# Kernel optimization log

Measured on AMD Instinct MI355X. Metric: run time of the kernel, lower is better.

The kernel has to match this reference:

```python
import jax, jax.numpy as jnp
import numpy as np

BS, L, D, CACHE = 8, 2048, 2048, 64   # sequences, tokens/seq, embed_dim, cache rows
T = BS * L
EPS = 1e-6


def setup_inputs() -> dict:
    key = jax.random.key(0)
    ks = jax.random.split(key, 7)
    inputs = jax.random.normal(ks[0], (T, D), jnp.float32)
    lf1_caches = jax.random.normal(ks[1], (CACHE, D), jnp.float32)
    lf2_caches = jax.random.normal(ks[2], (CACHE, D // 2), jnp.float32)
    conv1_weight = jax.random.normal(ks[3], (D, D), jnp.float32) * 0.02
    conv2_weight = jax.random.normal(ks[4], (D // 2, 2 * D), jnp.float32) * 0.02
    conv1_bias = jax.random.normal(ks[5], (D // 2,), jnp.float32) * 0.02
    conv2_bias = jax.random.normal(ks[6], (D,), jnp.float32) * 0.02
    ln_weight = jnp.ones((D,), jnp.float32)
    # consistent continuous-batching layout: each sequence s occupies rows
    # [s*(L+1) .. s*(L+1)+L] of the padded buffer: [cache_tok, tok0..tok_{L-1}]
    s = np.arange(BS, dtype=np.int64)
    j = np.arange(L, dtype=np.int64)
    pre_lf_indexs = jnp.asarray(s)                                  # cache slot per seq
    out_lf_indexs = jnp.asarray(s)
    input_lf_loc = jnp.asarray(s * (L + 1))                         # where cache row goes
    out_lf_loc = jnp.asarray(s * (L + 1) + L)                       # last token -> cache
    inputs_loc = jnp.asarray((s[:, None] * (L + 1) + 1 + j[None, :]).reshape(-1))
    outputs_loc = jnp.asarray((s[:, None] * (L + 1) + j[None, :]).reshape(-1))
    return {
        "inputs": inputs, "pre_lf_indexs": pre_lf_indexs, "out_lf_indexs": out_lf_indexs,
        "input_lf_loc": input_lf_loc, "out_lf_loc": out_lf_loc,
        "inputs_loc": inputs_loc, "outputs_loc": outputs_loc,
        "lf1_caches": lf1_caches, "lf2_caches": lf2_caches,
        "conv1_weight": conv1_weight, "conv2_weight": conv2_weight,
        "conv1_bias": conv1_bias, "conv2_bias": conv2_bias, "ln_weight": ln_weight,
    }


def _fused_cat_conv2d(x, cache, pre_idx, in_lf_loc, in_loc, out_loc, W):
    # scatter tokens + gathered cache rows into padded buffer [T+bs, d]
    bs = pre_idx.shape[0]
    xt = jnp.zeros((x.shape[0] + bs, x.shape[1]), x.dtype)
    xt = xt.at[in_loc].set(x).at[in_lf_loc].set(cache[pre_idx])
    c = xt @ W                                  # [T+bs, 2h]
    h = c.shape[1] // 2
    y = c[:-1, :h] + c[1:, h:]                  # kernel-2 causal conv via shift-add
    return y[out_loc]                           # [T, h]


def reference(inputs, pre_lf_indexs, out_lf_indexs, input_lf_loc, out_lf_loc,
              inputs_loc, outputs_loc, lf1_caches, lf2_caches,
              conv1_weight, conv2_weight, conv1_bias, conv2_bias, ln_weight):
    o1 = _fused_cat_conv2d(inputs, lf1_caches, pre_lf_indexs, input_lf_loc,
                           inputs_loc, outputs_loc, conv1_weight) + conv1_bias
    o2 = _fused_cat_conv2d(o1, lf2_caches, pre_lf_indexs, input_lf_loc,
                           inputs_loc, outputs_loc, conv2_weight) + conv2_bias
    o3 = o2 + inputs
    var = jnp.mean(o3 * o3, axis=-1, keepdims=True)          # RMSNorm
    return o3 * jax.lax.rsqrt(var + EPS) * ln_weight
```

## Files before the change

kernel.cpp:

```cpp
#include <hip/hip_runtime.h>
#include <hip/hip_bf16.h>
#include <stdint.h>

#define T_TOK   16384
#define BSQ     8
#define D1      2048
#define D2      1024

typedef __attribute__((ext_vector_type(8))) short bf16x8;
typedef __attribute__((ext_vector_type(4))) float f32x4;

__device__ __forceinline__ void gll16(const void* g, void* l) {
  __builtin_amdgcn_global_load_lds(
      (const __attribute__((address_space(1))) void*)g,
      (__attribute__((address_space(3))) void*)l, 16, 0, 0);
}

__global__ __launch_bounds__(256) void transpose_all(
    const float* __restrict__ W1, const float* __restrict__ W2,
    __hip_bfloat16* __restrict__ bt1, __hip_bfloat16* __restrict__ bt2) {
  __shared__ float tile[32][33];
  int job = blockIdx.x >> 11;
  int i = blockIdx.x & 2047;
  const float* in; __hip_bfloat16* out;
  int Cin, ldout, c0, kout0, bx, by;
  if (job < 2) {
    in = W1; out = bt1; Cin = 2048; ldout = 4096;
    c0 = job ? 1024 : 0; kout0 = job ? 2048 : 0;
    bx = (i & 31) * 32; by = (i >> 5) * 32;
  } else {
    in = W2; out = bt2; Cin = 4096; ldout = 2048;
    c0 = (job == 3) ? 2048 : 0; kout0 = (job == 3) ? 1024 : 0;
    bx = (i & 63) * 32; by = (i >> 6) * 32;
  }
  int tx = threadIdx.x, ty = threadIdx.y;
  #pragma unroll
  for (int q = 0; q < 32; q += 8)
    tile[ty + q][tx] = in[(size_t)(by + ty + q) * Cin + c0 + bx + tx];
  __syncthreads();
  #pragma unroll
  for (int q = 0; q < 32; q += 8)
    out[(size_t)(bx + ty + q) * ldout + kout0 + by + tx] =
        __float2bfloat16(tile[tx][ty + q]);
}

__global__ __launch_bounds__(256) void prologue(
    const float* __restrict__ x, const int* __restrict__ loc,
    const float* __restrict__ lf1, const float* __restrict__ lf2,
    const int* __restrict__ pre, const int* __restrict__ lfloc,
    __hip_bfloat16* __restrict__ xt1, __hip_bfloat16* __restrict__ xt2) {
  int b = blockIdx.x;
  if (b < T_TOK) {
    int c = threadIdx.x * 8;
    int r = loc[b];
    const float* src = x + (size_t)b * 2048 + c;
    float4 v0 = *(const float4*)src;
    float4 v1 = *(const float4*)(src + 4);
    union { __hip_bfloat16 h[8]; uint4 u; } o;
    o.h[0] = __float2bfloat16(v0.x); o.h[1] = __float2bfloat16(v0.y);
    o.h[2] = __float2bfloat16(v0.z); o.h[3] = __float2bfloat16(v0.w);
    o.h[4] = __float2bfloat16(v1.x); o.h[5] = __float2bfloat16(v1.y);
    o.h[6] = __float2bfloat16(v1.z); o.h[7] = __float2bfloat16(v1.w);
    *(uint4*)(xt1 + (size_t)r * 2048 + c) = o.u;
  } else if (b < T_TOK + BSQ) {
    int s = b - T_TOK;
    int dst = lfloc[s];
    const float* src = lf1 + (size_t)pre[s] * 2048;
    for (int c = threadIdx.x; c < 2048; c += 256)
      xt1[(size_t)dst * 2048 + c] = __float2bfloat16(src[c]);
  } else {
    int s = b - T_TOK - BSQ;
    int dst = lfloc[s];
    const float* src = lf2 + (size_t)pre[s] * 1024;
    for (int c = threadIdx.x; c < 1024; c += 256)
      xt2[(size_t)dst * 1024 + c] = __float2bfloat16(src[c]);
  }
}

template <int EPI>
__global__ __launch_bounds__(512, 2) void gemm_conv256(
    const __hip_bfloat16* __restrict__ A0,
    const __hip_bfloat16* __restrict__ Bt,
    const float* __restrict__ bias,
    const float* __restrict__ resid,
    __hip_bfloat16* __restrict__ outb,
    float* __restrict__ outf,
    int N, int K, int KH, int ldA, int tnBits) {
  extern __shared__ char smem[];
  const int tid = threadIdx.x;
  const int wave = tid >> 6, lane = tid & 63;
  const int wm = wave & 1, wn = wave >> 1;

  const int nwg = gridDim.x;
  const int bid = blockIdx.x;
  const int lb = (bid & 7) * (nwg >> 3) + (bid >> 3);
  const int tn = lb & ((1 << tnBits) - 1);
  const int tm = lb >> tnBits;

  const int s = tm >> 3;
  const size_t r0 = (size_t)tm * 256 + s;
  const int NTH = KH >> 6;
  const int NT = NTH * 2;

  const __hip_bfloat16* Bb = Bt + (size_t)tn * 256 * K;

  const int rloc = tid >> 3;
  const int c8 = (((tid & 7) ^ (rloc & 7)) << 3);

  const int frow = lane & 15;
  const int xr = (lane & 7) << 3;
  const int fk = (lane >> 4) << 3;
  const int ek0 = fk ^ xr;
  const int ek1 = (fk | 32) ^ xr;
  int aoff[8], boff[4];
  #pragma unroll
  for (int i = 0; i < 8; ++i) aoff[i] = (wm * 128 + i * 16 + frow) * 64;
  #pragma unroll
  for (int j = 0; j < 4; ++j) boff[j] = (wn * 64 + j * 16 + frow) * 64;

  f32x4 acc[8][4];
  #pragma unroll
  for (int i = 0; i < 8; ++i)
    #pragma unroll
    for (int j = 0; j < 4; ++j)
      #pragma unroll
      for (int e = 0; e < 4; ++e) acc[i][j][e] = 0.0f;

  auto stage = [&](int buf, int t) {
    int seg = (t >= NTH) ? 1 : 0;
    int kk = (t - (seg ? NTH : 0)) << 6;
    const __hip_bfloat16* Ar = A0 + (r0 + seg) * (size_t)ldA + kk + c8;
    const __hip_bfloat16* Bs = Bb + (seg ? KH : 0) + kk + c8;
    char* sbase = smem + buf * 65536 + wave * 1024;
    #pragma unroll
    for (int h = 0; h < 2; ++h)
      #pragma unroll
      for (int l = 0; l < 2; ++l) {
        int grow = h * 128 + l * 64 + rloc;
        gll16(Ar + (size_t)grow * ldA, sbase + h * 16384 + l * 8192);
        gll16(Bs + (size_t)grow * K,   sbase + 32768 + h * 16384 + l * 8192);
      }
  };

  stage(0, 0);
  stage(1, 1);
  asm volatile("s_waitcnt vmcnt(8)" ::: "memory");
  __builtin_amdgcn_s_barrier();
  asm volatile("" ::: "memory");

  #pragma unroll 1
  for (int t = 0; t < NT; t += 2) {
    #pragma unroll
    for (int half = 0; half < 2; ++half) {
      const int tt = t + half;
      const __hip_bfloat16* sT = (const __hip_bfloat16*)(smem + half * 65536);
      const __hip_bfloat16* sB = sT + 16384;

      __builtin_amdgcn_s_setprio(1);
      #pragma unroll
      for (int k = 0; k < 2; ++k) {
        const int ek = k ? ek1 : ek0;
        bf16x8 b[4], a[8];
        #pragma unroll
        for (int j = 0; j < 4; ++j) b[j] = *(const bf16x8*)(sB + boff[j] + ek);
        #pragma unroll
        for (int i = 0; i < 8; ++i) a[i] = *(const bf16x8*)(sT + aoff[i] + ek);
        #pragma unroll
        for (int i = 0; i < 8; ++i)
          #pragma unroll
          for (int j = 0; j < 4; ++j)
            acc[i][j] = __builtin_amdgcn_mfma_f32_16x16x32_bf16(
                a[i], b[j], acc[i][j], 0, 0, 0);
      }
      __builtin_amdgcn_s_setprio(0);

      asm volatile("s_waitcnt lgkmcnt(0)" ::: "memory");
      __builtin_amdgcn_s_barrier();
      asm volatile("" ::: "memory");

      if (tt + 2 < NT) {
        stage(half, tt + 2);
        __builtin_amdgcn_sched_barrier(0);
        asm volatile("s_waitcnt vmcnt(8)" ::: "memory");
      } else {
        asm volatile("s_waitcnt vmcnt(0)" ::: "memory");
      }
      __builtin_amdgcn_s_barrier();
      asm volatile("" ::: "memory");
    }
  }

  const int t0 = tm * 256 + wm * 128 + ((lane >> 4) << 2);
  const int ccol = tn * 256 + wn * 64 + (lane & 15);
  float bj[4];
  #pragma unroll
  for (int j = 0; j < 4; ++j) bj[j] = bias[ccol + j * 16];

  #pragma unroll
  for (int i = 0; i < 8; ++i)
    #pragma unroll
    for (int p = 0; p < 4; ++p) {
      int tk = t0 + i * 16 + p;
      if (EPI == 1) {
        __hip_bfloat16* dst = outb + ((size_t)tk + s + 1) * N + ccol;
        #pragma unroll
        for (int j = 0; j < 4; ++j)
          dst[j * 16] = __float2bfloat16(acc[i][j][p] + bj[j]);
      } else {
        const float* rsrc = resid + (size_t)tk * N + ccol;
        float* dst = outf + (size_t)tk * N + ccol;
        #pragma unroll
        for (int j = 0; j < 4; ++j)
          dst[j * 16] = acc[i][j][p] + bj[j] + rsrc[j * 16];
      }
    }
}

__global__ __launch_bounds__(256) void rmsnorm(
    const float* __restrict__ o3, const float* __restrict__ lnw,
    float* __restrict__ out) {
  __shared__ float red[4];
  int t = blockIdx.x;
  int d = threadIdx.x * 8;
  const float* p = o3 + (size_t)t * 2048 + d;
  float o[8];
  *(float4*)&o[0] = *(const float4*)p;
  *(float4*)&o[4] = *(const float4*)(p + 4);
  float ss = 0.0f;
  #pragma unroll
  for (int k = 0; k < 8; ++k) ss += o[k] * o[k];
  #pragma unroll
  for (int off = 32; off > 0; off >>= 1) ss += __shfl_down(ss, off, 64);
  if ((threadIdx.x & 63) == 0) red[threadIdx.x >> 6] = ss;
  __syncthreads();
  float tot = red[0] + red[1] + red[2] + red[3];
  float sc = rsqrtf(tot * (1.0f / 2048.0f) + 1e-6f);
  float lw[8], res[8];
  *(float4*)&lw[0] = *(const float4*)(lnw + d);
  *(float4*)&lw[4] = *(const float4*)(lnw + d + 4);
  #pragma unroll
  for (int k = 0; k < 8; ++k) res[k] = o[k] * sc * lw[k];
  float* dst = out + (size_t)t * 2048 + d;
  *(float4*)dst = *(float4*)&res[0];
  *(float4*)(dst + 4) = *(float4*)&res[4];
}

extern "C" void kernel_launch(void* const* d_in, const int* in_sizes, int n_in,
                              void* d_out, int out_size, void* d_ws, size_t ws_size,
                              hipStream_t stream) {
  const float* inputs = (const float*)d_in[0];
  const int* pre_idx  = (const int*)d_in[1];
  const int* in_lf_loc = (const int*)d_in[3];
  const int* in_loc  = (const int*)d_in[5];
  const float* lf1 = (const float*)d_in[7];
  const float* lf2 = (const float*)d_in[8];
  const float* W1 = (const float*)d_in[9];
  const float* W2 = (const float*)d_in[10];
  const float* b1 = (const float*)d_in[11];
  const float* b2 = (const float*)d_in[12];
  const float* lnw = (const float*)d_in[13];
  float* out = (float*)d_out;

  char* ws = (char*)d_ws;
  float* o3 = (float*)ws;
  __hip_bfloat16* xt1 = (__hip_bfloat16*)(ws + 134217728ull);
  __hip_bfloat16* xt2 = (__hip_bfloat16*)(ws + 201359360ull);
  __hip_bfloat16* bt1 = (__hip_bfloat16*)(ws + 234930176ull);
  __hip_bfloat16* bt2 = (__hip_bfloat16*)(ws + 243318784ull);

  static int lds_inited = 0;
  if (!lds_inited) {
    lds_inited = 1;
    (void)hipFuncSetAttribute(reinterpret_cast<const void*>(&gemm_conv256<1>),
                              hipFuncAttributeMaxDynamicSharedMemorySize, 131072);
    (void)hipFuncSetAttribute(reinterpret_cast<const void*>(&gemm_conv256<2>),
                              hipFuncAttributeMaxDynamicSharedMemorySize, 131072);
  }

  transpose_all<<<8192, dim3(32, 8), 0, stream>>>(W1, W2, bt1, bt2);
  prologue<<<T_TOK + 2 * BSQ, 256, 0, stream>>>(
      inputs, in_loc, lf1, lf2, pre_idx, in_lf_loc, xt1, xt2);

  gemm_conv256<1><<<256, 512, 131072, stream>>>(
      xt1, bt1, b1, nullptr, xt2, nullptr, 1024, 4096, 2048, 2048, 2);

  gemm_conv256<2><<<512, 512, 131072, stream>>>(
      xt2, bt2, b2, inputs, nullptr, o3, 2048, 2048, 1024, 1024, 3);

  rmsnorm<<<T_TOK, 256, 0, stream>>>(o3, lnw, out);
}
```

Before: 575.8 us.

## Restructure GEMM main loop into finer-grained interleaved load/compute phases

Splits each K-tile's compute into four sub-phases of 16 MFMAs. The global-to-LDS staging of the next tile's A and B quarters is issued between them, with barriers around each sub-phase, in the style of an 8-wave ping-pong schedule. The aim is to spread memory traffic across the compute and hide load latency better than the previous two-stage all-at-once staging. In exchange it adds many more barriers per iteration and tighter vmcnt waits, which could serialize waves if the overlap does not pay off.

```diff
diff --git a/kernel.cpp b/kernel.cpp
--- a/kernel.cpp
+++ b/kernel.cpp
@@ -107,6 +107,29 @@
   const int rloc = tid >> 3;
   const int c8 = (((tid & 7) ^ (rloc & 7)) << 3);
 
+  auto stageA = [&](int buf, int t, int qsel) {
+    int seg = (t >= NTH) ? 1 : 0;
+    int kk = (t - (seg ? NTH : 0)) << 6;
+    const __hip_bfloat16* Ar = A0 + (r0 + seg) * (size_t)ldA + kk + c8;
+    char* sb = smem + buf * 65536 + (size_t)(qsel * 64 + wave * 8) * 128;
+    #pragma unroll
+    for (int l = 0; l < 2; ++l) {
+      int grow = l * 128 + qsel * 64 + rloc;
+      gll16(Ar + (size_t)grow * ldA, sb + l * 16384);
+    }
+  };
+  auto stageB = [&](int buf, int t, int hsel) {
+    int seg = (t >= NTH) ? 1 : 0;
+    int kk = (t - (seg ? NTH : 0)) << 6;
+    const __hip_bfloat16* Bs = Bb + (seg ? KH : 0) + kk + c8;
+    char* sb = smem + buf * 65536 + 32768 + (size_t)(hsel * 128 + wave * 8) * 128;
+    #pragma unroll
+    for (int l = 0; l < 2; ++l) {
+      int grow = hsel * 128 + l * 64 + rloc;
+      gll16(Bs + (size_t)grow * K, sb + l * 8192);
+    }
+  };
+
   const int frow = lane & 15;
   const int xr = (lane & 7) << 3;
   const int fk = (lane >> 4) << 3;
@@ -126,68 +149,99 @@
       #pragma unroll
       for (int e = 0; e < 4; ++e) acc[i][j][e] = 0.0f;
 
-  auto stage = [&](int buf, int t) {
-    int seg = (t >= NTH) ? 1 : 0;
-    int kk = (t - (seg ? NTH : 0)) << 6;
-    const __hip_bfloat16* Ar = A0 + (r0 + seg) * (size_t)ldA + kk + c8;
-    const __hip_bfloat16* Bs = Bb + (seg ? KH : 0) + kk + c8;
-    char* sbase = smem + buf * 65536 + wave * 1024;
-    #pragma unroll
-    for (int h = 0; h < 2; ++h)
-      #pragma unroll
-      for (int l = 0; l < 2; ++l) {
-        int grow = h * 128 + l * 64 + rloc;
-        gll16(Ar + (size_t)grow * ldA, sbase + h * 16384 + l * 8192);
-        gll16(Bs + (size_t)grow * K,   sbase + 32768 + h * 16384 + l * 8192);
-      }
-  };
-
-  stage(0, 0);
-  stage(1, 1);
-  asm volatile("s_waitcnt vmcnt(8)" ::: "memory");
+  stageA(0, 0, 0);
+  stageA(0, 0, 1);
+  stageB(0, 0, 0);
+  stageB(0, 0, 1);
+  stageA(1, 1, 0);
+  asm volatile("s_waitcnt vmcnt(2)" ::: "memory");
   __builtin_amdgcn_s_barrier();
   asm volatile("" ::: "memory");
 
   #pragma unroll 1
-  for (int t = 0; t < NT; t += 2) {
-    #pragma unroll
-    for (int half = 0; half < 2; ++half) {
-      const int tt = t + half;
-      const __hip_bfloat16* sT = (const __hip_bfloat16*)(smem + half * 65536);
-      const __hip_bfloat16* sB = sT + 16384;
-
-      __builtin_amdgcn_s_setprio(1);
-      #pragma unroll
-      for (int k = 0; k < 2; ++k) {
-        const int ek = k ? ek1 : ek0;
-        bf16x8 b[4], a[8];
-        #pragma unroll
-        for (int j = 0; j < 4; ++j) b[j] = *(const bf16x8*)(sB + boff[j] + ek);
-        #pragma unroll
-        for (int i = 0; i < 8; ++i) a[i] = *(const bf16x8*)(sT + aoff[i] + ek);
-        #pragma unroll
-        for (int i = 0; i < 8; ++i)
-          #pragma unroll
-          for (int j = 0; j < 4; ++j)
-            acc[i][j] = __builtin_amdgcn_mfma_f32_16x16x32_bf16(
-                a[i], b[j], acc[i][j], 0, 0, 0);
-      }
-      __builtin_amdgcn_s_setprio(0);
-
-      asm volatile("s_waitcnt lgkmcnt(0)" ::: "memory");
-      __builtin_amdgcn_s_barrier();
-      asm volatile("" ::: "memory");
-
-      if (tt + 2 < NT) {
-        stage(half, tt + 2);
-        __builtin_amdgcn_sched_barrier(0);
-        asm volatile("s_waitcnt vmcnt(8)" ::: "memory");
-      } else {
-        asm volatile("s_waitcnt vmcnt(0)" ::: "memory");
-      }
-      __builtin_amdgcn_s_barrier();
-      asm volatile("" ::: "memory");
-    }
+  for (int v = 0; v < NT; ++v) {
+    const int p = v & 1;
+    const __hip_bfloat16* sA_ = (const __hip_bfloat16*)(smem + p * 65536);
+    const __hip_bfloat16* sB_ = sA_ + 16384;
+    bf16x8 a[4], b[4];
+
+    #pragma unroll
+    for (int j = 0; j < 4; ++j) b[j] = *(const bf16x8*)(sB_ + boff[j] + ek0);
+    #pragma unroll
+    for (int i = 0; i < 4; ++i) a[i] = *(const bf16x8*)(sA_ + aoff[i] + ek0);
+    if (v + 1 < NT) stageA(p ^ 1, v + 1, 1);
+    asm volatile("" ::: "memory");
+    __builtin_amdgcn_s_barrier();
+    asm volatile("s_waitcnt lgkmcnt(0)" ::: "memory");
+    __builtin_amdgcn_sched_barrier(0);
+    __builtin_amdgcn_s_setprio(1);
+    #pragma unroll
+    for (int i = 0; i < 4; ++i)
+      #pragma unroll
+      for (int j = 0; j < 4; ++j)
+        acc[i][j] = __builtin_amdgcn_mfma_f32_16x16x32_bf16(a[i], b[j], acc[i][j], 0, 0, 0);
+    __builtin_amdgcn_s_setprio(0);
+    asm volatile("" ::: "memory");
+    __builtin_amdgcn_s_barrier();
+    asm volatile("" ::: "memory");
+
+    #pragma unroll
+    for (int i = 0; i < 4; ++i) a[i] = *(const bf16x8*)(sA_ + aoff[4 + i] + ek0);
+    if (v + 1 < NT) stageB(p ^ 1, v + 1, 0);
+    asm volatile("" ::: "memory");
+    __builtin_amdgcn_s_barrier();
+    asm volatile("s_waitcnt lgkmcnt(0)" ::: "memory");
+    __builtin_amdgcn_sched_barrier(0);
+    __builtin_amdgcn_s_setprio(1);
+    #pragma unroll
+    for (int i = 0; i < 4; ++i)
+      #pragma unroll
+      for (int j = 0; j < 4; ++j)
+        acc[4 + i][j] = __builtin_amdgcn_mfma_f32_16x16x32_bf16(a[i], b[j], acc[4 + i][j], 0, 0, 0);
+    __builtin_amdgcn_s_setprio(0);
+    asm volatile("" ::: "memory");
+    __builtin_amdgcn_s_barrier();
+    asm volatile("" ::: "memory");
+
+    #pragma unroll
+    for (int j = 0; j < 4; ++j) b[j] = *(const bf16x8*)(sB_ + boff[j] + ek1);
+    #pragma unroll
+    for (int i = 0; i < 4; ++i) a[i] = *(const bf16x8*)(sA_ + aoff[i] + ek1);
+    if (v + 1 < NT) stageB(p ^ 1, v + 1, 1);
+    asm volatile("" ::: "memory");
+    __builtin_amdgcn_s_barrier();
+    asm volatile("s_waitcnt lgkmcnt(0)" ::: "memory");
+    __builtin_amdgcn_sched_barrier(0);
+    __builtin_amdgcn_s_setprio(1);
+    #pragma unroll
+    for (int i = 0; i < 4; ++i)
+      #pragma unroll
+      for (int j = 0; j < 4; ++j)
+        acc[i][j] = __builtin_amdgcn_mfma_f32_16x16x32_bf16(a[i], b[j], acc[i][j], 0, 0, 0);
+    __builtin_amdgcn_s_setprio(0);
+    asm volatile("" ::: "memory");
+    __builtin_amdgcn_s_barrier();
+    asm volatile("" ::: "memory");
+
+    #pragma unroll
+    for (int i = 0; i < 4; ++i) a[i] = *(const bf16x8*)(sA_ + aoff[4 + i] + ek1);
+    if (v + 2 < NT) stageA(p, v + 2, 0);
+    __builtin_amdgcn_sched_barrier(0);
+    if (v < NT - 2) { asm volatile("s_waitcnt vmcnt(2)" ::: "memory"); }
+    else            { asm volatile("s_waitcnt vmcnt(0)" ::: "memory"); }
+    __builtin_amdgcn_s_barrier();
+    asm volatile("s_waitcnt lgkmcnt(0)" ::: "memory");
+    __builtin_amdgcn_sched_barrier(0);
+    __builtin_amdgcn_s_setprio(1);
+    #pragma unroll
+    for (int i = 0; i < 4; ++i)
+      #pragma unroll
+      for (int j = 0; j < 4; ++j)
+        acc[4 + i][j] = __builtin_amdgcn_mfma_f32_16x16x32_bf16(a[i], b[j], acc[4 + i][j], 0, 0, 0);
+    __builtin_amdgcn_s_setprio(0);
+    asm volatile("" ::: "memory");
+    __builtin_amdgcn_s_barrier();
+    asm volatile("" ::: "memory");
   }
 
   const int t0 = tm * 256 + wm * 128 + ((lane >> 4) << 2);
```

Measured after the change: 605.8 us. 5.2% more time.

## Software-pipeline LDS fragment reads against MFMA in GEMM main loop

Applied to the files above, without the earlier changes.

Restructures the GEMM inner loop so LDS fragment reads for the next sub-block are issued while MFMAs on the current sub-block run, splitting A into two M-halves and prefetching the first fragments of the next K tile before the loop iteration ends. Global-to-LDS staging is split into A and B helpers and issued mid-iteration, overlapping with the last MFMA group. This aims to hide LDS read latency behind matrix math. In exchange it raises register pressure from more live fragment buffers and drops the setprio hints.

```diff
diff --git a/kernel.cpp b/kernel.cpp
--- a/kernel.cpp
+++ b/kernel.cpp
@@ -107,6 +107,29 @@
   const int rloc = tid >> 3;
   const int c8 = (((tid & 7) ^ (rloc & 7)) << 3);
 
+  auto stageA = [&](int buf, int t, int qsel) {
+    int seg = (t >= NTH) ? 1 : 0;
+    int kk = (t - (seg ? NTH : 0)) << 6;
+    const __hip_bfloat16* Ar = A0 + (r0 + seg) * (size_t)ldA + kk + c8;
+    char* sb = smem + buf * 65536 + (size_t)(qsel * 64 + wave * 8) * 128;
+    #pragma unroll
+    for (int l = 0; l < 2; ++l) {
+      int grow = l * 128 + qsel * 64 + rloc;
+      gll16(Ar + (size_t)grow * ldA, sb + l * 16384);
+    }
+  };
+  auto stageB = [&](int buf, int t, int hsel) {
+    int seg = (t >= NTH) ? 1 : 0;
+    int kk = (t - (seg ? NTH : 0)) << 6;
+    const __hip_bfloat16* Bs = Bb + (seg ? KH : 0) + kk + c8;
+    char* sb = smem + buf * 65536 + 32768 + (size_t)(hsel * 128 + wave * 8) * 128;
+    #pragma unroll
+    for (int l = 0; l < 2; ++l) {
+      int grow = hsel * 128 + l * 64 + rloc;
+      gll16(Bs + (size_t)grow * K, sb + l * 8192);
+    }
+  };
+
   const int frow = lane & 15;
   const int xr = (lane & 7) << 3;
   const int fk = (lane >> 4) << 3;
@@ -126,67 +149,71 @@
       #pragma unroll
       for (int e = 0; e < 4; ++e) acc[i][j][e] = 0.0f;
 
-  auto stage = [&](int buf, int t) {
-    int seg = (t >= NTH) ? 1 : 0;
-    int kk = (t - (seg ? NTH : 0)) << 6;
-    const __hip_bfloat16* Ar = A0 + (r0 + seg) * (size_t)ldA + kk + c8;
-    const __hip_bfloat16* Bs = Bb + (seg ? KH : 0) + kk + c8;
-    char* sbase = smem + buf * 65536 + wave * 1024;
-    #pragma unroll
-    for (int h = 0; h < 2; ++h)
+  bf16x8 a0[4], a1[4], a2[4], a3[4], b0[4], b1[4];
+
+  auto rdA = [&](bf16x8* d, const __hip_bfloat16* base, int mh, int ek) {
+    #pragma unroll
+    for (int i = 0; i < 4; ++i)
+      d[i] = *(const bf16x8*)(base + aoff[mh * 4 + i] + ek);
+  };
+  auto rdB = [&](bf16x8* d, const __hip_bfloat16* base, int ek) {
+    #pragma unroll
+    for (int j = 0; j < 4; ++j)
+      d[j] = *(const bf16x8*)(base + boff[j] + ek);
+  };
+  auto mm = [&](int mh, const bf16x8* a, const bf16x8* b) {
+    #pragma unroll
+    for (int i = 0; i < 4; ++i)
       #pragma unroll
-      for (int l = 0; l < 2; ++l) {
-        int grow = h * 128 + l * 64 + rloc;
-        gll16(Ar + (size_t)grow * ldA, sbase + h * 16384 + l * 8192);
-        gll16(Bs + (size_t)grow * K,   sbase + 32768 + h * 16384 + l * 8192);
-      }
-  };
-
-  stage(0, 0);
-  stage(1, 1);
+      for (int j = 0; j < 4; ++j)
+        acc[mh * 4 + i][j] = __builtin_amdgcn_mfma_f32_16x16x32_bf16(
+            a[i], b[j], acc[mh * 4 + i][j], 0, 0, 0);
+  };
+
+  stageA(0, 0, 0); stageA(0, 0, 1); stageB(0, 0, 0); stageB(0, 0, 1);
+  stageA(1, 1, 0); stageA(1, 1, 1); stageB(1, 1, 0); stageB(1, 1, 1);
   asm volatile("s_waitcnt vmcnt(8)" ::: "memory");
   __builtin_amdgcn_s_barrier();
   asm volatile("" ::: "memory");
 
+  const __hip_bfloat16* sA_ = (const __hip_bfloat16*)smem;
+  const __hip_bfloat16* sB_ = sA_ + 16384;
+  rdB(b0, sB_, ek0);
+  rdA(a0, sA_, 0, ek0);
+
   #pragma unroll 1
-  for (int t = 0; t < NT; t += 2) {
-    #pragma unroll
-    for (int half = 0; half < 2; ++half) {
-      const int tt = t + half;
-      const __hip_bfloat16* sT = (const __hip_bfloat16*)(smem + half * 65536);
-      const __hip_bfloat16* sB = sT + 16384;
-
-      __builtin_amdgcn_s_setprio(1);
-      #pragma unroll
-      for (int k = 0; k < 2; ++k) {
-        const int ek = k ? ek1 : ek0;
-        bf16x8 b[4], a[8];
-        #pragma unroll
-        for (int j = 0; j < 4; ++j) b[j] = *(const bf16x8*)(sB + boff[j] + ek);
-        #pragma unroll
-        for (int i = 0; i < 8; ++i) a[i] = *(const bf16x8*)(sT + aoff[i] + ek);
-        #pragma unroll
-        for (int i = 0; i < 8; ++i)
-          #pragma unroll
-          for (int j = 0; j < 4; ++j)
-            acc[i][j] = __builtin_amdgcn_mfma_f32_16x16x32_bf16(
-                a[i], b[j], acc[i][j], 0, 0, 0);
-      }
-      __builtin_amdgcn_s_setprio(0);
-
-      asm volatile("s_waitcnt lgkmcnt(0)" ::: "memory");
+  for (int v = 0; v < NT; ++v) {
+    const int p = v & 1;
+
+    rdA(a1, sA_, 1, ek0);
+    mm(0, a0, b0);
+
+    rdB(b1, sB_, ek1);
+    rdA(a2, sA_, 0, ek1);
+    mm(1, a1, b0);
+
+    rdA(a3, sA_, 1, ek1);
+    mm(0, a2, b1);
+
+    asm volatile("s_waitcnt lgkmcnt(0)" ::: "memory");
+    __builtin_amdgcn_s_barrier();
+    asm volatile("" ::: "memory");
+
+    if (v + 2 < NT) {
+      stageA(p, v + 2, 0); stageA(p, v + 2, 1);
+      stageB(p, v + 2, 0); stageB(p, v + 2, 1);
+    }
+    mm(1, a3, b1);
+
+    if (v + 1 < NT) {
+      if (v + 2 < NT) { asm volatile("s_waitcnt vmcnt(8)" ::: "memory"); }
+      else            { asm volatile("s_waitcnt vmcnt(0)" ::: "memory"); }
       __builtin_amdgcn_s_barrier();
       asm volatile("" ::: "memory");
-
-      if (tt + 2 < NT) {
-        stage(half, tt + 2);
-        __builtin_amdgcn_sched_barrier(0);
-        asm volatile("s_waitcnt vmcnt(8)" ::: "memory");
-      } else {
-        asm volatile("s_waitcnt vmcnt(0)" ::: "memory");
-      }
-      __builtin_amdgcn_s_barrier();
-      asm volatile("" ::: "memory");
+      sA_ = (const __hip_bfloat16*)(smem + (p ^ 1) * 65536);
+      sB_ = sA_ + 16384;
+      rdB(b0, sB_, ek0);
+      rdA(a0, sA_, 0, ek0);
     }
   }
 
```

Result: no change. 573.8 us (-0.4%).

## Restructure GEMM to 128x256 tiles with triple-buffered K=32 stages

Applied to the files above, without the earlier changes.

The conv GEMM now uses 256-thread workgroups with 128x256 output tiles and a K step of 32, and twice as many workgroups are launched. LDS goes from two 64 KB buffers to three 24 KB stages with a 3-deep load pipeline, and each stage's fragments are prefetched into registers before the next MFMA loop. The swizzle pattern and per-wave fragment layout are rewritten to match. The aim is better occupancy and latency hiding from the smaller LDS footprint and more workgroups, at the cost of more barriers per unit of K and less reuse per tile.

```diff
diff --git a/kernel.cpp b/kernel.cpp
--- a/kernel.cpp
+++ b/kernel.cpp
@@ -78,7 +78,7 @@
 }
 
 template <int EPI>
-__global__ __launch_bounds__(512, 2) void gemm_conv256(
+__global__ __launch_bounds__(256, 2) void gemm_conv128(
     const __hip_bfloat16* __restrict__ A0,
     const __hip_bfloat16* __restrict__ Bt,
     const float* __restrict__ bias,
@@ -97,120 +97,118 @@
   const int tn = lb & ((1 << tnBits) - 1);
   const int tm = lb >> tnBits;
 
-  const int s = tm >> 3;
-  const size_t r0 = (size_t)tm * 256 + s;
-  const int NTH = KH >> 6;
+  const int s = tm >> 4;
+  const size_t r0 = (size_t)tm * 128 + s;
+  const int NTH = KH >> 5;
   const int NT = NTH * 2;
 
   const __hip_bfloat16* Bb = Bt + (size_t)tn * 256 * K;
 
-  const int rloc = tid >> 3;
-  const int c8 = (((tid & 7) ^ (rloc & 7)) << 3);
+  const int rloc = tid >> 2;
+  const int c8 = (((tid & 3) ^ ((tid >> 3) & 3)) << 3);
+  const int ldsb = wave * 1024;
+
+  auto stage = [&](char* dst, int t) {
+    int seg = (t >= NTH) ? 1 : 0;
+    int kk = (t - (seg ? NTH : 0)) << 5;
+    const __hip_bfloat16* Ar = A0 + (r0 + seg) * (size_t)ldA + kk + c8;
+    const __hip_bfloat16* Bs = Bb + (seg ? KH : 0) + kk + c8;
+    #pragma unroll
+    for (int l = 0; l < 2; ++l)
+      gll16(Ar + (size_t)(l * 64 + rloc) * ldA, dst + l * 4096 + ldsb);
+    #pragma unroll
+    for (int l = 0; l < 4; ++l)
+      gll16(Bs + (size_t)(l * 64 + rloc) * K, dst + 8192 + l * 4096 + ldsb);
+  };
 
   const int frow = lane & 15;
-  const int xr = (lane & 7) << 3;
-  const int fk = (lane >> 4) << 3;
-  const int ek0 = fk ^ xr;
-  const int ek1 = (fk | 32) ^ xr;
-  int aoff[8], boff[4];
-  #pragma unroll
-  for (int i = 0; i < 8; ++i) aoff[i] = (wm * 128 + i * 16 + frow) * 64;
-  #pragma unroll
-  for (int j = 0; j < 4; ++j) boff[j] = (wn * 64 + j * 16 + frow) * 64;
-
-  f32x4 acc[8][4];
-  #pragma unroll
-  for (int i = 0; i < 8; ++i)
-    #pragma unroll
-    for (int j = 0; j < 4; ++j)
+  const int ek = (((lane >> 4) ^ ((frow >> 1) & 3)) << 3);
+  int aoff[4], boff[8];
+  #pragma unroll
+  for (int i = 0; i < 4; ++i) aoff[i] = (wm * 64 + i * 16 + frow) * 32;
+  #pragma unroll
+  for (int j = 0; j < 8; ++j) boff[j] = (wn * 128 + j * 16 + frow) * 32;
+
+  f32x4 acc[4][8];
+  #pragma unroll
+  for (int i = 0; i < 4; ++i)
+    #pragma unroll
+    for (int j = 0; j < 8; ++j)
       #pragma unroll
       for (int e = 0; e < 4; ++e) acc[i][j][e] = 0.0f;
 
-  auto stage = [&](int buf, int t) {
-    int seg = (t >= NTH) ? 1 : 0;
-    int kk = (t - (seg ? NTH : 0)) << 6;
-    const __hip_bfloat16* Ar = A0 + (r0 + seg) * (size_t)ldA + kk + c8;
-    const __hip_bfloat16* Bs = Bb + (seg ? KH : 0) + kk + c8;
-    char* sbase = smem + buf * 65536 + wave * 1024;
-    #pragma unroll
-    for (int h = 0; h < 2; ++h)
-      #pragma unroll
-      for (int l = 0; l < 2; ++l) {
-        int grow = h * 128 + l * 64 + rloc;
-        gll16(Ar + (size_t)grow * ldA, sbase + h * 16384 + l * 8192);
-        gll16(Bs + (size_t)grow * K,   sbase + 32768 + h * 16384 + l * 8192);
-      }
+  bf16x8 a[4], b[8];
+  auto rdfr = [&](const char* buf) {
+    const __hip_bfloat16* a_ = (const __hip_bfloat16*)buf;
+    const __hip_bfloat16* b_ = (const __hip_bfloat16*)(buf + 8192);
+    #pragma unroll
+    for (int i = 0; i < 4; ++i) a[i] = *(const bf16x8*)(a_ + aoff[i] + ek);
+    #pragma unroll
+    for (int j = 0; j < 8; ++j) b[j] = *(const bf16x8*)(b_ + boff[j] + ek);
   };
 
-  stage(0, 0);
-  stage(1, 1);
-  asm volatile("s_waitcnt vmcnt(8)" ::: "memory");
+  char* s0 = smem;
+  char* s1 = smem + 24576;
+  char* s2 = smem + 49152;
+  stage(s0, 0); stage(s1, 1); stage(s2, 2);
+  asm volatile("s_waitcnt vmcnt(12)" ::: "memory");
   __builtin_amdgcn_s_barrier();
   asm volatile("" ::: "memory");
+  rdfr(s0);
+
+  char* cb = s0;
+  char* nb = s1;
+  char* tb = s2;
 
   #pragma unroll 1
-  for (int t = 0; t < NT; t += 2) {
-    #pragma unroll
-    for (int half = 0; half < 2; ++half) {
-      const int tt = t + half;
-      const __hip_bfloat16* sT = (const __hip_bfloat16*)(smem + half * 65536);
-      const __hip_bfloat16* sB = sT + 16384;
-
-      __builtin_amdgcn_s_setprio(1);
+  for (int v = 0; v < NT; ++v) {
+    __builtin_amdgcn_s_setprio(1);
+    #pragma unroll
+    for (int i = 0; i < 4; ++i)
       #pragma unroll
-      for (int k = 0; k < 2; ++k) {
-        const int ek = k ? ek1 : ek0;
-        bf16x8 b[4], a[8];
-        #pragma unroll
-        for (int j = 0; j < 4; ++j) b[j] = *(const bf16x8*)(sB + boff[j] + ek);
-        #pragma unroll
-        for (int i = 0; i < 8; ++i) a[i] = *(const bf16x8*)(sT + aoff[i] + ek);
-        #pragma unroll
-        for (int i = 0; i < 8; ++i)
-          #pragma unroll
-          for (int j = 0; j < 4; ++j)
-            acc[i][j] = __builtin_amdgcn_mfma_f32_16x16x32_bf16(
-                a[i], b[j], acc[i][j], 0, 0, 0);
-      }
-      __builtin_amdgcn_s_setprio(0);
-
-      asm volatile("s_waitcnt lgkmcnt(0)" ::: "memory");
+      for (int j = 0; j < 8; ++j)
+        acc[i][j] = __builtin_amdgcn_mfma_f32_16x16x32_bf16(
+            a[i], b[j], acc[i][j], 0, 0, 0);
+    __builtin_amdgcn_s_setprio(0);
+
+    asm volatile("s_waitcnt lgkmcnt(0)" ::: "memory");
+    __builtin_amdgcn_s_barrier();
+    asm volatile("" ::: "memory");
+
+    if (v + 3 < NT) stage(cb, v + 3);
+
+    if (v + 1 < NT) {
+      if (v + 3 < NT)      { asm volatile("s_waitcnt vmcnt(12)" ::: "memory"); }
+      else if (v + 2 < NT) { asm volatile("s_waitcnt vmcnt(6)" ::: "memory"); }
+      else                 { asm volatile("s_waitcnt vmcnt(0)" ::: "memory"); }
       __builtin_amdgcn_s_barrier();
       asm volatile("" ::: "memory");
-
-      if (tt + 2 < NT) {
-        stage(half, tt + 2);
-        __builtin_amdgcn_sched_barrier(0);
-        asm volatile("s_waitcnt vmcnt(8)" ::: "memory");
-      } else {
-        asm volatile("s_waitcnt vmcnt(0)" ::: "memory");
-      }
-      __builtin_amdgcn_s_barrier();
-      asm volatile("" ::: "memory");
+      rdfr(nb);
     }
-  }
-
-  const int t0 = tm * 256 + wm * 128 + ((lane >> 4) << 2);
-  const int ccol = tn * 256 + wn * 64 + (lane & 15);
-  float bj[4];
-  #pragma unroll
-  for (int j = 0; j < 4; ++j) bj[j] = bias[ccol + j * 16];
-
-  #pragma unroll
-  for (int i = 0; i < 8; ++i)
+    char* rot = cb; cb = nb; nb = tb; tb = rot;
+  }
+
+  const int t0 = tm * 128 + wm * 64 + ((lane >> 4) << 2);
+  const int ccol = tn * 256 + wn * 128 + (lane & 15);
+  float bj[8];
+  #pragma unroll
+  for (int j = 0; j < 8; ++j) bj[j] = bias[ccol + j * 16];
+
+  #pragma unroll
+  for (int i = 0; i < 4; ++i)
     #pragma unroll
     for (int p = 0; p < 4; ++p) {
       int tk = t0 + i * 16 + p;
       if (EPI == 1) {
         __hip_bfloat16* dst = outb + ((size_t)tk + s + 1) * N + ccol;
         #pragma unroll
-        for (int j = 0; j < 4; ++j)
+        for (int j = 0; j < 8; ++j)
           dst[j * 16] = __float2bfloat16(acc[i][j][p] + bj[j]);
       } else {
         const float* rsrc = resid + (size_t)tk * N + ccol;
         float* dst = outf + (size_t)tk * N + ccol;
         #pragma unroll
-        for (int j = 0; j < 4; ++j)
+        for (int j = 0; j < 8; ++j)
           dst[j * 16] = acc[i][j][p] + bj[j] + rsrc[j * 16];
       }
     }
@@ -271,20 +269,20 @@
   static int lds_inited = 0;
   if (!lds_inited) {
     lds_inited = 1;
-    (void)hipFuncSetAttribute(reinterpret_cast<const void*>(&gemm_conv256<1>),
-                              hipFuncAttributeMaxDynamicSharedMemorySize, 131072);
-    (void)hipFuncSetAttribute(reinterpret_cast<const void*>(&gemm_conv256<2>),
-                              hipFuncAttributeMaxDynamicSharedMemorySize, 131072);
+    (void)hipFuncSetAttribute(reinterpret_cast<const void*>(&gemm_conv128<1>),
+                              hipFuncAttributeMaxDynamicSharedMemorySize, 73728);
+    (void)hipFuncSetAttribute(reinterpret_cast<const void*>(&gemm_conv128<2>),
+                              hipFuncAttributeMaxDynamicSharedMemorySize, 73728);
   }
 
   transpose_all<<<8192, dim3(32, 8), 0, stream>>>(W1, W2, bt1, bt2);
   prologue<<<T_TOK + 2 * BSQ, 256, 0, stream>>>(
       inputs, in_loc, lf1, lf2, pre_idx, in_lf_loc, xt1, xt2);
 
-  gemm_conv256<1><<<256, 512, 131072, stream>>>(
+  gemm_conv128<1><<<512, 256, 73728, stream>>>(
       xt1, bt1, b1, nullptr, xt2, nullptr, 1024, 4096, 2048, 2048, 2);
 
-  gemm_conv256<2><<<512, 512, 131072, stream>>>(
+  gemm_conv128<2><<<1024, 256, 73728, stream>>>(
       xt2, bt2, b2, inputs, nullptr, o3, 2048, 2048, 1024, 1024, 3);
 
   rmsnorm<<<T_TOK, 256, 0, stream>>>(o3, lnw, out);
```

Result: slower. 595.7 us (+3.4%).
